# Optimization experiments

Measured on AMD Instinct MI355X. Metric: run time of the kernel, lower is better.

Reference implementation:

```python
import jax, jax.numpy as jnp
import numpy as np

RAY_START, RAY_END, BOX_SIZE = 0.0, 1.0, 2.0
EPS = 1e-10


def grid_sample_bilinear(img, grid):
    """Replicates F.grid_sample(mode='bilinear', padding_mode='zeros', align_corners=True).
    img: [N, F, H, W]; grid: [N, P, 2] with (x, y) in [-1, 1] (x indexes W, y indexes H).
    Returns [N, F, P]."""
    H, W = img.shape[2], img.shape[3]
    x = (grid[..., 0] + 1.0) * 0.5 * (W - 1)  # [N, P]
    y = (grid[..., 1] + 1.0) * 0.5 * (H - 1)
    x0 = jnp.floor(x).astype(jnp.int32)
    y0 = jnp.floor(y).astype(jnp.int32)
    x1, y1 = x0 + 1, y0 + 1
    wx = x - x0.astype(x.dtype)
    wy = y - y0.astype(y.dtype)

    def gather(ix, iy):
        valid = ((ix >= 0) & (ix < W) & (iy >= 0) & (iy < H)).astype(img.dtype)
        ixc = jnp.clip(ix, 0, W - 1)
        iyc = jnp.clip(iy, 0, H - 1)
        v = jax.vmap(lambda im, jx, jy: im[:, jy, jx])(img, ixc, iyc)  # [N, F, P]
        return v * valid[:, None, :]

    return (gather(x0, y0) * ((1 - wx) * (1 - wy))[:, None, :]
            + gather(x1, y0) * (wx * (1 - wy))[:, None, :]
            + gather(x0, y1) * ((1 - wx) * wy)[:, None, :]
            + gather(x1, y1) * (wx * wy)[:, None, :])


def setup_inputs() -> dict:
    key = jax.random.key(0)
    ks = jax.random.split(key, 6)
    B, R, N, F, HP, HID = 2, 4096, 48, 32, 256, 64
    planes = jax.random.normal(ks[0], (B, 3, F, HP, HP), jnp.float32)
    ray_origins = jax.random.normal(ks[1], (B, R, 3), jnp.float32) * 0.05
    rd = jax.random.normal(ks[2], (B, R, 3), jnp.float32)
    ray_directions = rd / jnp.linalg.norm(rd, axis=-1, keepdims=True)
    jitter = jax.random.uniform(ks[3], (B, R, N, 1), jnp.float32)
    W1 = jax.random.normal(ks[4], (F, HID), jnp.float32) * 0.1
    b1 = jnp.zeros((HID,), jnp.float32)
    W2 = jax.random.normal(ks[5], (HID, 4), jnp.float32) * 0.1
    b2 = jnp.zeros((4,), jnp.float32)
    return dict(planes=planes, ray_origins=ray_origins, ray_directions=ray_directions,
                jitter=jitter, W1=W1, b1=b1, W2=W2, b2=b2)


def reference(planes, ray_origins, ray_directions, jitter, W1, b1, W2, b2):
    B, R, N, _ = jitter.shape
    F_, HP, WP = planes.shape[2], planes.shape[3], planes.shape[4]
    P = R * N

    # sample_stratified over normalized s in [0, 1], jittered (EG3D style)
    steps = jnp.arange(N, dtype=jnp.float32) / (N - 1)          # [N]
    s_delta = 1.0 / (N - 1)
    sdist = steps.reshape(1, 1, N, 1) + jitter * s_delta         # [B, R, N, 1]
    tdist = sdist * RAY_END + (1.0 - sdist) * RAY_START          # s_to_t

    # world-space sample coordinates -> tri-plane lookup
    coords = ray_origins[:, :, None, :] + tdist * ray_directions[:, :, None, :]  # [B,R,N,3]
    coords = coords.reshape(B, P, 3) / (BOX_SIZE / 2.0)
    c2d = jnp.stack([coords[..., (0, 1)], coords[..., (0, 2)], coords[..., (1, 2)]],
                    axis=1).reshape(B * 3, P, 2)
    feats = grid_sample_bilinear(planes.reshape(B * 3, F_, HP, WP), c2d)  # [B*3, F, P]
    feats = feats.reshape(B, 3, F_, P).transpose(0, 1, 3, 2)              # [B, 3, P, F]

    # OSGDecoder-style MLP: mean over planes, Linear -> softplus -> Linear
    x = feats.mean(axis=1)                      # [B, P, F]
    h = jax.nn.softplus(x @ W1 + b1)            # [B, P, HID]
    o = h @ W2 + b2                             # [B, P, 4]
    sigma = o[..., :1].reshape(B, R, N, 1)
    rgb = (jax.nn.sigmoid(o[..., 1:]) * 1.002 - 0.001).reshape(B, R, N, 3)

    # ClassicalRayMarcher (clamp_mode='softplus', cut_quantile=0, use_inf_depth=True)
    deltas = sdist[:, :, 1:] - sdist[:, :, :-1]
    deltas = jnp.concatenate([deltas, jnp.full_like(deltas[:, :, :1], 1e10)], axis=2)
    dens = jax.nn.softplus(sigma)
    alphas = 1.0 - jnp.exp(-deltas * dens)                     # [B, R, N, 1]
    T = jnp.cumprod(1.0 - alphas + EPS, axis=2)
    T = jnp.concatenate([jnp.ones_like(T[:, :, :1]), T], axis=2)  # [B, R, N+1, 1]
    final_transmittance = T[:, :, -1, 0]                       # [B, R]
    weights = alphas * T[:, :, :-1]                            # [B, R, N, 1]
    rgb_final = jnp.sum(weights * rgb, axis=2)                 # [B, R, 3]
    depth = jnp.sum(weights * sdist, axis=2)                   # [B, R, 1]
    return rgb_final, depth, weights.sum(axis=2), final_transmittance
```

## Files before the change

kernel.cpp:

```cpp
#include <hip/hip_runtime.h>
#include <hip/hip_fp16.h>
#include <math.h>

#define BATCH 2
#define RAYS  4096
#define NS    48
#define FEAT  32
#define HP    256
#define HID   64
#define NRAY  (BATCH*RAYS)
#define NSAMP (NRAY*NS)
#define S_DELTA (1.0f/47.0f)

typedef unsigned short u16;
typedef __attribute__((ext_vector_type(8))) _Float16 half8;
typedef __attribute__((ext_vector_type(4))) float facc4;

__device__ __forceinline__ float softplus_f(float t) {
    float e = __expf(-fabsf(t));
    return fmaxf(t, 0.0f) + __logf(1.0f + e);
}
__device__ __forceinline__ float sigmoid_f(float t) {
    return 1.0f / (1.0f + __expf(-t));
}

__global__ __launch_bounds__(256)
void prep_kernel(const float* __restrict__ planes,
                 const float* __restrict__ W1,
                 const float* __restrict__ W2,
                 u16* __restrict__ pT,
                 u16* __restrict__ W1F,
                 u16* __restrict__ W2F) {
    int idx = blockIdx.x * 256 + threadIdx.x;
    const int total = BATCH * 3 * HP * HP;
    if (idx < total) {
        int xy = idx % (HP * HP);
        int bp = idx / (HP * HP);
        const float* src = planes + (size_t)bp * FEAT * HP * HP + xy;
        unsigned o16[16];
        #pragma unroll
        for (int k = 0; k < 16; ++k) {
            unsigned lo = __half_as_ushort(__float2half_rn(src[(size_t)(2*k)   * HP*HP]));
            unsigned hi = __half_as_ushort(__float2half_rn(src[(size_t)(2*k+1) * HP*HP]));
            o16[k] = lo | (hi << 16);
        }
        uint4* dst = (uint4*)(pT + (size_t)idx * FEAT);
        #pragma unroll
        for (int q = 0; q < 4; ++q)
            dst[q] = make_uint4(o16[4*q], o16[4*q+1], o16[4*q+2], o16[4*q+3]);
    } else {
        int r = idx - total;
        #pragma unroll
        for (int i = 0; i < 8; ++i) {
            int e = r * 8 + i;
            int nt = e >> 9, ll = (e >> 3) & 63, ii = e & 7;
            int k = ((ll >> 4) << 3) + ii;
            int nn = (nt << 4) + (ll & 15);
            W1F[e] = __half_as_ushort(__float2half_rn(W1[k * HID + nn] * (1.f/3.f)));
        }
        if (r < 128) {
            #pragma unroll
            for (int i = 0; i < 8; ++i) {
                int e = r * 8 + i;
                int kk = e >> 9, ll = (e >> 3) & 63, ii = e & 7;
                int k = kk * 32 + ((ll >> 4) << 3) + ii;
                int nn = ll & 15;
                W2F[e] = (nn < 4) ? __half_as_ushort(__float2half_rn(W2[k * 4 + nn]))
                                  : (u16)0;
            }
        }
    }
}

__device__ __forceinline__ void corner_f16(const u16* __restrict__ p,
                                           float w, __half2 acc[4]) {
    union { uint4 q; __half2 h[4]; } U;
    U.q = *(const uint4*)p;
    __half2 w2 = __float2half2_rn(w);
    #pragma unroll
    for (int i = 0; i < 4; ++i)
        acc[i] = __hfma2(U.h[i], w2, acc[i]);
}

__device__ __forceinline__ void gather_plane_f16(const u16* __restrict__ pb,
                                                 float gx, float gy, int fc8,
                                                 __half2 acc[4]) {
    float px = (gx + 1.0f) * 0.5f * (float)(HP - 1);
    float py = (gy + 1.0f) * 0.5f * (float)(HP - 1);
    float fx = floorf(px), fy = floorf(py);
    float wx = px - fx, wy = py - fy;
    int x0 = (int)fx, y0 = (int)fy;
    int x1 = x0 + 1, y1 = y0 + 1;
    bool vx0 = (unsigned)x0 < HP, vx1 = (unsigned)x1 < HP;
    bool vy0 = (unsigned)y0 < HP, vy1 = (unsigned)y1 < HP;
    int cx0 = min(max(x0, 0), HP-1), cx1 = min(max(x1, 0), HP-1);
    int cy0 = min(max(y0, 0), HP-1), cy1 = min(max(y1, 0), HP-1);
    float w00 = (vx0 && vy0) ? (1.f-wx)*(1.f-wy) : 0.f;
    float w10 = (vx1 && vy0) ? wx*(1.f-wy)       : 0.f;
    float w01 = (vx0 && vy1) ? (1.f-wx)*wy       : 0.f;
    float w11 = (vx1 && vy1) ? wx*wy             : 0.f;
    corner_f16(pb + ((size_t)(cy0*HP + cx0)*FEAT + fc8), w00, acc);
    corner_f16(pb + ((size_t)(cy0*HP + cx1)*FEAT + fc8), w10, acc);
    corner_f16(pb + ((size_t)(cy1*HP + cx0)*FEAT + fc8), w01, acc);
    corner_f16(pb + ((size_t)(cy1*HP + cx1)*FEAT + fc8), w11, acc);
}

__global__ __launch_bounds__(768, 6)
void render_mfma(const u16* __restrict__ pT,
                 const float* __restrict__ rayo,
                 const float* __restrict__ rayd,
                 const float* __restrict__ jitter,
                 const u16* __restrict__ W1F,
                 const u16* __restrict__ W2F,
                 const float* __restrict__ b1,
                 const float* __restrict__ b2,
                 float* __restrict__ out) {
    __shared__ __align__(16) u16 hlds[12][1024];
    __shared__ __align__(16) float4 s_smp[192];
    __shared__ float s_sd[192];

    const int t = threadIdx.x;
    const int w = t >> 6;
    const int l = t & 63;
    const int c = l & 15;
    const int g = l >> 4;
    const int S0 = blockIdx.x * 192;
    const int ls = w * 16 + c;
    const int s  = S0 + ls;
    const int ray = s / NS;
    const int n = s - ray * NS;
    const int b = ray >> 12;

    const float jit = jitter[s];
    const float sd = fmaf((float)n, S_DELTA, jit * S_DELTA);
    const float ox = rayo[ray*3+0], oy = rayo[ray*3+1], oz = rayo[ray*3+2];
    const float dx = rayd[ray*3+0], dy = rayd[ray*3+1], dz = rayd[ray*3+2];
    const float cxv = fmaf(sd, dx, ox);
    const float cyv = fmaf(sd, dy, oy);
    const float czv = fmaf(sd, dz, oz);

    __half2 acc[4];
    #pragma unroll
    for (int i = 0; i < 4; ++i) acc[i] = __float2half2_rn(0.f);

    const int fc8 = g * 8;
    const u16* base = pT + (size_t)b * 3 * HP * HP * FEAT;
    gather_plane_f16(base,                         cxv, cyv, fc8, acc);
    gather_plane_f16(base + (size_t)HP*HP*FEAT,    cxv, czv, fc8, acc);
    gather_plane_f16(base + 2*(size_t)HP*HP*FEAT,  cyv, czv, fc8, acc);

    union { __half2 h[4]; half8 v; } A;
    #pragma unroll
    for (int i = 0; i < 4; ++i) A.h[i] = acc[i];

    const facc4 z4 = {0.f, 0.f, 0.f, 0.f};
    facc4 H[4];
    #pragma unroll
    for (int nt = 0; nt < 4; ++nt) {
        union { uint4 q; half8 v; } B;
        B.q = *(const uint4*)(W1F + (size_t)(nt * 64 + l) * 8);
        H[nt] = __builtin_amdgcn_mfma_f32_16x16x32_f16(A.v, B.v, z4, 0, 0, 0);
    }

    char* lb = (char*)&hlds[w][0];
    #pragma unroll
    for (int nt = 0; nt < 4; ++nt) {
        const float bb = b1[nt * 16 + c];
        #pragma unroll
        for (int r = 0; r < 4; ++r) {
            const int row = g * 4 + r;
            const float hv = softplus_f(H[nt][r] + bb);
            const int off = row * 128 + ((((nt * 16 + c) * 2)) ^ ((row & 7) << 4));
            *(u16*)(lb + off) = __half_as_ushort(__float2half_rn(hv));
        }
    }

    facc4 O = z4;
    #pragma unroll
    for (int kk = 0; kk < 2; ++kk) {
        union { uint4 q; half8 v; } A2;
        const int off = c * 128 + ((kk * 64 + g * 16) ^ ((c & 7) << 4));
        A2.q = *(const uint4*)(lb + off);
        union { uint4 q; half8 v; } B2;
        B2.q = *(const uint4*)(W2F + (size_t)(kk * 64 + l) * 8);
        O = __builtin_amdgcn_mfma_f32_16x16x32_f16(A2.v, B2.v, O, 0, 0, 0);
    }

    if (c < 4) {
        const float bb = b2[c];
        #pragma unroll
        for (int r = 0; r < 4; ++r) {
            const int li = w * 16 + g * 4 + r;
            const float o = O[r] + bb;
            const float val = (c == 0) ? softplus_f(o)
                                       : (sigmoid_f(o) * 1.002f - 0.001f);
            ((float*)&s_smp[li])[c] = val;
        }
    }
    if (g == 0) s_sd[ls] = sd;
    __syncthreads();

    if (w < 4) {
        const int rray = blockIdx.x * 4 + w;
        const bool valid = l < NS;
        float4 v = make_float4(0.f, 0.f, 0.f, 0.f);
        float sdc = 0.f;
        if (valid) { v = s_smp[w * NS + l]; sdc = s_sd[w * NS + l]; }
        float sdn = __shfl_down(sdc, 1);

        float alpha = 0.f, lg = 0.f;
        if (valid) {
            float delta = (l < NS - 1) ? (sdn - sdc) : 1e10f;
            float tt = __expf(-delta * v.x);
            alpha = 1.0f - tt;
            lg = __logf(tt + 1e-10f);
        }
        float sacc = lg;
        #pragma unroll
        for (int off = 1; off < 64; off <<= 1) {
            float u = __shfl_up(sacc, off);
            if (l >= off) sacc += u;
        }
        float finalLog = __shfl(sacc, NS - 1);
        float T   = __expf(sacc - lg);
        float wgt = valid ? alpha * T : 0.f;

        float rf = wgt * v.y, gf = wgt * v.z, bf = wgt * v.w;
        float dep = wgt * sdc, wsum = wgt;
        #pragma unroll
        for (int off = 32; off; off >>= 1) {
            rf   += __shfl_xor(rf, off);
            gf   += __shfl_xor(gf, off);
            bf   += __shfl_xor(bf, off);
            dep  += __shfl_xor(dep, off);
            wsum += __shfl_xor(wsum, off);
        }
        if (l == 0) {
            out[rray * 3 + 0] = rf;
            out[rray * 3 + 1] = gf;
            out[rray * 3 + 2] = bf;
            out[NRAY * 3 + rray] = dep;
            out[NRAY * 4 + rray] = wsum;
            out[NRAY * 5 + rray] = __expf(finalLog);
        }
    }
}

__global__ __launch_bounds__(192)
void render_fused(const float* __restrict__ pl,
                  const float* __restrict__ rayo,
                  const float* __restrict__ rayd,
                  const float* __restrict__ jitter,
                  const float* __restrict__ W1, const float* __restrict__ b1,
                  const float* __restrict__ W2, const float* __restrict__ b2,
                  float* __restrict__ out) {
    __shared__ float4 smpb[192];
    __shared__ float  sdsb[192];
    int tid = threadIdx.x;
    int lr  = tid / NS;
    int n   = tid - lr * NS;
    int ray = blockIdx.x * 4 + lr;
    int b   = ray >> 12;

    float jit = jitter[ray * NS + n];
    float sd  = (float)n * S_DELTA + jit * S_DELTA;
    float ox = rayo[ray*3+0], oy = rayo[ray*3+1], oz = rayo[ray*3+2];
    float dx = rayd[ray*3+0], dy = rayd[ray*3+1], dz = rayd[ray*3+2];
    float cx = fmaf(sd, dx, ox), cy = fmaf(sd, dy, oy), cz = fmaf(sd, dz, oz);

    float xv[32];
    #pragma unroll
    for (int i = 0; i < 32; ++i) xv[i] = 0.f;
    const size_t psz = (size_t)HP * HP * FEAT;
    const float* base = pl + (size_t)b * 3 * psz;
    float gxs[3] = {cx, cx, cy}, gys[3] = {cy, cz, cz};
    for (int p = 0; p < 3; ++p) {
        float px = (gxs[p] + 1.0f) * 0.5f * (float)(HP - 1);
        float py = (gys[p] + 1.0f) * 0.5f * (float)(HP - 1);
        float fx = floorf(px), fy = floorf(py);
        float wx = px - fx, wy = py - fy;
        int x0 = (int)fx, y0 = (int)fy, x1 = x0 + 1, y1 = y0 + 1;
        const float* pb = base + p * psz;
        float ws[4] = {(1.f-wx)*(1.f-wy), wx*(1.f-wy), (1.f-wx)*wy, wx*wy};
        int xs[4] = {x0, x1, x0, x1}, ys[4] = {y0, y0, y1, y1};
        for (int q = 0; q < 4; ++q) {
            if ((unsigned)xs[q] < HP && (unsigned)ys[q] < HP) {
                const float* pp = pb + (size_t)ys[q] * HP + xs[q];
                #pragma unroll
                for (int f = 0; f < 32; ++f)
                    xv[f] = fmaf(ws[q], pp[(size_t)f * HP * HP], xv[f]);
            }
        }
    }
    #pragma unroll
    for (int i = 0; i < 32; ++i) xv[i] *= (1.f/3.f);

    float o0 = b2[0], o1 = b2[1], o2 = b2[2], o3 = b2[3];
    #pragma unroll
    for (int j = 0; j < HID; ++j) {
        float hj = b1[j];
        #pragma unroll
        for (int f = 0; f < FEAT; ++f) hj = fmaf(xv[f], W1[f * HID + j], hj);
        hj = softplus_f(hj);
        o0 = fmaf(hj, W2[j*4+0], o0);
        o1 = fmaf(hj, W2[j*4+1], o1);
        o2 = fmaf(hj, W2[j*4+2], o2);
        o3 = fmaf(hj, W2[j*4+3], o3);
    }
    smpb[tid] = make_float4(softplus_f(o0),
                            sigmoid_f(o1) * 1.002f - 0.001f,
                            sigmoid_f(o2) * 1.002f - 0.001f,
                            sigmoid_f(o3) * 1.002f - 0.001f);
    sdsb[tid] = sd;
    __syncthreads();

    if (tid < 4) {
        int rray = blockIdx.x * 4 + tid;
        const float4* sp  = &smpb[tid * NS];
        const float*  sdp = &sdsb[tid * NS];
        float T = 1.0f, rf = 0.f, gf = 0.f, bfv = 0.f, dep = 0.f, wsum = 0.f;
        for (int m = 0; m < NS; ++m) {
            float4 vv = sp[m];
            float sdc = sdp[m];
            float delta = (m < NS - 1) ? (sdp[m+1] - sdc) : 1e10f;
            float alpha = 1.0f - __expf(-delta * vv.x);
            float wq = alpha * T;
            rf = fmaf(wq, vv.y, rf);
            gf = fmaf(wq, vv.z, gf);
            bfv = fmaf(wq, vv.w, bfv);
            dep = fmaf(wq, sdc, dep);
            wsum += wq;
            T *= (1.0f - alpha + 1e-10f);
        }
        out[rray*3+0] = rf;
        out[rray*3+1] = gf;
        out[rray*3+2] = bfv;
        out[NRAY*3 + rray] = dep;
        out[NRAY*4 + rray] = wsum;
        out[NRAY*5 + rray] = T;
    }
}

extern "C" void kernel_launch(void* const* d_in, const int* in_sizes, int n_in,
                              void* d_out, int out_size, void* d_ws, size_t ws_size,
                              hipStream_t stream) {
    const float* planes = (const float*)d_in[0];
    const float* rayo   = (const float*)d_in[1];
    const float* rayd   = (const float*)d_in[2];
    const float* jitter = (const float*)d_in[3];
    const float* W1     = (const float*)d_in[4];
    const float* b1     = (const float*)d_in[5];
    const float* W2     = (const float*)d_in[6];
    const float* b2     = (const float*)d_in[7];
    float* out = (float*)d_out;

    const size_t pT_bytes = (size_t)BATCH * 3 * HP * HP * FEAT * 2;
    const size_t w1f_off  = pT_bytes;
    const size_t w2f_off  = w1f_off + (size_t)FEAT * HID * 2;
    const size_t need     = w2f_off + (size_t)HID * 16 * 2;

    if (ws_size >= need) {
        char* ws = (char*)d_ws;
        u16* pT  = (u16*)ws;
        u16* W1F = (u16*)(ws + w1f_off);
        u16* W2F = (u16*)(ws + w2f_off);
        const int tgrid = BATCH * 3 * HP * HP / 256 + 1;
        hipLaunchKernelGGL(prep_kernel, dim3(tgrid), dim3(256), 0, stream,
                           planes, W1, W2, pT, W1F, W2F);
        hipLaunchKernelGGL(render_mfma, dim3(NSAMP / 192), dim3(768), 0, stream,
                           pT, rayo, rayd, jitter, W1F, W2F, b1, b2, out);
    } else {
        hipLaunchKernelGGL(render_fused, dim3(NRAY / 4), dim3(192), 0, stream,
                           planes, rayo, rayd, jitter, W1, b1, W2, b2, out);
    }
}
```

Baseline: 60.11 us.

## Use one 192-thread block per ray, fold biases into MFMA accumulators

The render kernel drops from 768-thread blocks covering four rays to 192-thread blocks covering a single ray. Only one wavefront per block now does the ray-marching scan, so the other waves no longer sit idle at the barrier and shared memory per block shrinks. Biases b1 and b2 are now loaded into the MFMA accumulator as its initial value instead of being added afterwards. Each plane's gather accumulates into its own half2 register set, and the three are summed at the end, which shortens dependency chains but uses more registers. The trade-off is four times as many blocks and a lower occupancy hint in launch_bounds.

```diff
diff --git a/kernel.cpp b/kernel.cpp
--- a/kernel.cpp
+++ b/kernel.cpp
@@ -105,7 +105,7 @@
     corner_f16(pb + ((size_t)(cy1*HP + cx1)*FEAT + fc8), w11, acc);
 }
 
-__global__ __launch_bounds__(768, 6)
+__global__ __launch_bounds__(192, 8)
 void render_mfma(const u16* __restrict__ pT,
                  const float* __restrict__ rayo,
                  const float* __restrict__ rayd,
@@ -115,67 +115,71 @@
                  const float* __restrict__ b1,
                  const float* __restrict__ b2,
                  float* __restrict__ out) {
-    __shared__ __align__(16) u16 hlds[12][1024];
-    __shared__ __align__(16) float4 s_smp[192];
-    __shared__ float s_sd[192];
+    __shared__ __align__(16) u16 hlds[3][1024];
+    __shared__ __align__(16) float4 s_smp[48];
+    __shared__ float s_sd[48];
 
     const int t = threadIdx.x;
     const int w = t >> 6;
     const int l = t & 63;
     const int c = l & 15;
     const int g = l >> 4;
-    const int S0 = blockIdx.x * 192;
+    const int ray = blockIdx.x;
     const int ls = w * 16 + c;
-    const int s  = S0 + ls;
-    const int ray = s / NS;
-    const int n = s - ray * NS;
-    const int b = ray >> 12;
+    const int s  = ray * NS + ls;
+    const int b  = ray >> 12;
 
     const float jit = jitter[s];
-    const float sd = fmaf((float)n, S_DELTA, jit * S_DELTA);
+    const float sd = fmaf((float)ls, S_DELTA, jit * S_DELTA);
     const float ox = rayo[ray*3+0], oy = rayo[ray*3+1], oz = rayo[ray*3+2];
     const float dx = rayd[ray*3+0], dy = rayd[ray*3+1], dz = rayd[ray*3+2];
     const float cxv = fmaf(sd, dx, ox);
     const float cyv = fmaf(sd, dy, oy);
     const float czv = fmaf(sd, dz, oz);
 
-    __half2 acc[4];
-    #pragma unroll
-    for (int i = 0; i < 4; ++i) acc[i] = __float2half2_rn(0.f);
+    __half2 a0[4], a1[4], a2[4];
+    #pragma unroll
+    for (int i = 0; i < 4; ++i) {
+        a0[i] = __float2half2_rn(0.f);
+        a1[i] = __float2half2_rn(0.f);
+        a2[i] = __float2half2_rn(0.f);
+    }
 
     const int fc8 = g * 8;
     const u16* base = pT + (size_t)b * 3 * HP * HP * FEAT;
-    gather_plane_f16(base,                         cxv, cyv, fc8, acc);
-    gather_plane_f16(base + (size_t)HP*HP*FEAT,    cxv, czv, fc8, acc);
-    gather_plane_f16(base + 2*(size_t)HP*HP*FEAT,  cyv, czv, fc8, acc);
+    gather_plane_f16(base,                         cxv, cyv, fc8, a0);
+    gather_plane_f16(base + (size_t)HP*HP*FEAT,    cxv, czv, fc8, a1);
+    gather_plane_f16(base + 2*(size_t)HP*HP*FEAT,  cyv, czv, fc8, a2);
 
     union { __half2 h[4]; half8 v; } A;
     #pragma unroll
-    for (int i = 0; i < 4; ++i) A.h[i] = acc[i];
-
-    const facc4 z4 = {0.f, 0.f, 0.f, 0.f};
+    for (int i = 0; i < 4; ++i)
+        A.h[i] = __hadd2(__hadd2(a0[i], a1[i]), a2[i]);
+
     facc4 H[4];
     #pragma unroll
     for (int nt = 0; nt < 4; ++nt) {
+        const float bb = b1[nt * 16 + c];
+        facc4 Cb = {bb, bb, bb, bb};
         union { uint4 q; half8 v; } B;
         B.q = *(const uint4*)(W1F + (size_t)(nt * 64 + l) * 8);
-        H[nt] = __builtin_amdgcn_mfma_f32_16x16x32_f16(A.v, B.v, z4, 0, 0, 0);
+        H[nt] = __builtin_amdgcn_mfma_f32_16x16x32_f16(A.v, B.v, Cb, 0, 0, 0);
     }
 
     char* lb = (char*)&hlds[w][0];
     #pragma unroll
     for (int nt = 0; nt < 4; ++nt) {
-        const float bb = b1[nt * 16 + c];
         #pragma unroll
         for (int r = 0; r < 4; ++r) {
             const int row = g * 4 + r;
-            const float hv = softplus_f(H[nt][r] + bb);
+            const float hv = softplus_f(H[nt][r]);
             const int off = row * 128 + ((((nt * 16 + c) * 2)) ^ ((row & 7) << 4));
             *(u16*)(lb + off) = __half_as_ushort(__float2half_rn(hv));
         }
     }
 
-    facc4 O = z4;
+    const float bb2 = b2[c & 3];
+    facc4 O = {bb2, bb2, bb2, bb2};
     #pragma unroll
     for (int kk = 0; kk < 2; ++kk) {
         union { uint4 q; half8 v; } A2;
@@ -187,11 +191,10 @@
     }
 
     if (c < 4) {
-        const float bb = b2[c];
         #pragma unroll
         for (int r = 0; r < 4; ++r) {
             const int li = w * 16 + g * 4 + r;
-            const float o = O[r] + bb;
+            const float o = O[r];
             const float val = (c == 0) ? softplus_f(o)
                                        : (sigmoid_f(o) * 1.002f - 0.001f);
             ((float*)&s_smp[li])[c] = val;
@@ -200,12 +203,11 @@
     if (g == 0) s_sd[ls] = sd;
     __syncthreads();
 
-    if (w < 4) {
-        const int rray = blockIdx.x * 4 + w;
+    if (w == 0) {
         const bool valid = l < NS;
         float4 v = make_float4(0.f, 0.f, 0.f, 0.f);
         float sdc = 0.f;
-        if (valid) { v = s_smp[w * NS + l]; sdc = s_sd[w * NS + l]; }
+        if (valid) { v = s_smp[l]; sdc = s_sd[l]; }
         float sdn = __shfl_down(sdc, 1);
 
         float alpha = 0.f, lg = 0.f;
@@ -236,12 +238,12 @@
             wsum += __shfl_xor(wsum, off);
         }
         if (l == 0) {
-            out[rray * 3 + 0] = rf;
-            out[rray * 3 + 1] = gf;
-            out[rray * 3 + 2] = bf;
-            out[NRAY * 3 + rray] = dep;
-            out[NRAY * 4 + rray] = wsum;
-            out[NRAY * 5 + rray] = __expf(finalLog);
+            out[ray * 3 + 0] = rf;
+            out[ray * 3 + 1] = gf;
+            out[ray * 3 + 2] = bf;
+            out[NRAY * 3 + ray] = dep;
+            out[NRAY * 4 + ray] = wsum;
+            out[NRAY * 5 + ray] = __expf(finalLog);
         }
     }
 }
@@ -367,7 +369,7 @@
         const int tgrid = BATCH * 3 * HP * HP / 256 + 1;
         hipLaunchKernelGGL(prep_kernel, dim3(tgrid), dim3(256), 0, stream,
                            planes, W1, W2, pT, W1F, W2F);
-        hipLaunchKernelGGL(render_mfma, dim3(NSAMP / 192), dim3(768), 0, stream,
+        hipLaunchKernelGGL(render_mfma, dim3(NRAY), dim3(192), 0, stream,
                            pT, rayo, rayd, jitter, W1F, W2F, b1, b2, out);
     } else {
         hipLaunchKernelGGL(render_fused, dim3(NRAY / 4), dim3(192), 0, stream,
```

Measured after the change: 58.47 us. 2.7% less time.
